# Performance work log

Measured on AMD Instinct MI355X. Metric: run time of the kernel, lower is better.

The kernel has to match this reference:

```python
import jax, jax.numpy as jnp
import numpy as np

E = 1024      # embed_dim
H = 16        # num_heads
D = E // H    # head_dim = 64
K = 4         # num_hyper_nodes
MAX_SEQ = 8192
ROPE_BASE = 10000.0
SCALE = D ** -0.5


def rotate_half(x):
    half = x.shape[-1] // 2
    return jnp.concatenate([-x[..., half:], x[..., :half]], axis=-1)


def _rope_cache():
    inv_freq = 1.0 / (ROPE_BASE ** (jnp.arange(0, D, 2, dtype=jnp.float32) / D))
    t = jnp.arange(MAX_SEQ, dtype=jnp.float32)
    freqs = jnp.outer(t, inv_freq)                       # (MAX_SEQ, D/2)
    emb = jnp.concatenate([freqs, freqs], axis=-1)       # (MAX_SEQ, D)
    return jnp.cos(emb), jnp.sin(emb)


def setup_inputs() -> dict:
    key = jax.random.key(0)
    ks = jax.random.split(key, 6)
    B, S = 2, 2048
    w_scale = E ** -0.5  # keep pre-softmax logits in a sane range
    return {
        "x":  jax.random.normal(ks[0], (B, S, E), dtype=jnp.float32),
        "Wq": jax.random.normal(ks[1], (E, E), dtype=jnp.float32) * w_scale,
        "Wk": jax.random.normal(ks[2], (E, E), dtype=jnp.float32) * w_scale,
        "Wv": jax.random.normal(ks[3], (E, E), dtype=jnp.float32) * w_scale,
        "Wr": jax.random.normal(ks[4], (E, H * K), dtype=jnp.float32) * w_scale,
        "Wo": jax.random.normal(ks[5], (E, E), dtype=jnp.float32) * w_scale,
    }


def reference(x, Wq, Wk, Wv, Wr, Wo):
    B, S, _ = x.shape
    # projections -> (B, H, S, D)
    q = (x @ Wq).reshape(B, S, H, D).transpose(0, 2, 1, 3)
    k = (x @ Wk).reshape(B, S, H, D).transpose(0, 2, 1, 3)
    v = (x @ Wv).reshape(B, S, H, D).transpose(0, 2, 1, 3)

    # node routing probabilities (B, H, S, K)
    logits = (x @ Wr).reshape(B, S, H, K).transpose(0, 2, 1, 3)
    node_probs = jax.nn.softmax(logits, axis=-1)

    # expected per-node position: sum_{j<i} p[j,k]  -> (B, H, S, K)
    expected_pos = jnp.cumsum(node_probs, axis=2) - node_probs

    # fractional-position RoPE via linear interpolation of the cos/sin cache
    cos_c, sin_c = _rope_cache()
    pos = jnp.clip(expected_pos, 0.0, MAX_SEQ - 1)
    pf = pos.astype(jnp.int32)                   # floor
    pc = jnp.minimum(pf + 1, MAX_SEQ - 1)        # ceil
    frac = (pos - pf.astype(pos.dtype))[..., None]
    cos = cos_c[pf] + frac * (cos_c[pc] - cos_c[pf])   # (B,H,S,K,D)
    sin = sin_c[pf] + frac * (sin_c[pc] - sin_c[pf])

    # Weighted combine over nodes. Since q_k = q*cos_k + rh(q)*sin_k is linear
    # in (cos_k, sin_k), sum_k p_k * q_k = q * (sum_k p_k cos_k) + rh(q) * (sum_k p_k sin_k)
    cos_w = jnp.einsum('bhsk,bhskd->bhsd', node_probs, cos)
    sin_w = jnp.einsum('bhsk,bhskd->bhsd', node_probs, sin)
    q_r = q * cos_w + rotate_half(q) * sin_w
    k_r = k * cos_w + rotate_half(k) * sin_w

    # P(same node) weights (B, H, S, S)
    node_w = jnp.einsum('bhik,bhjk->bhij', node_probs, node_probs)

    scores = jnp.einsum('bhid,bhjd->bhij', q_r, k_r) * SCALE
    scores = scores + jnp.log(node_w + 1e-8)
    causal = jnp.tril(jnp.ones((S, S), dtype=bool))
    scores = jnp.where(causal[None, None], scores, -jnp.inf)
    attn = jax.nn.softmax(scores, axis=-1)

    out = jnp.einsum('bhij,bhjd->bhid', attn, v)
    out = out.transpose(0, 2, 1, 3).reshape(B, S, E)
    return out @ Wo
```

## Files before the change

### kernel.cpp

```cpp
#include <hip/hip_runtime.h>

#define E_ 1024
#define H_ 16
#define D_ 64
#define K_ 4
#define S_ 2048
#define B_ 2
#define BS_ 4096
#define BH_ 32
#define CT_ 2080

typedef __attribute__((ext_vector_type(8))) short short8;
typedef __attribute__((ext_vector_type(4))) float f32x4;
typedef __attribute__((ext_vector_type(4))) unsigned short u16x4;

__device__ __forceinline__ unsigned short f2bf(float f) {
  union { float f; unsigned u; } v; v.f = f;
  unsigned r = v.u + 0x7FFFu + ((v.u >> 16) & 1u);
  return (unsigned short)(r >> 16);
}
__device__ __forceinline__ float bf2f(unsigned short u) {
  union { unsigned u; float f; } v; v.u = ((unsigned)u) << 16; return v.f;
}

typedef __attribute__((address_space(1))) const void gvoid;
typedef __attribute__((address_space(3))) void lvoid;
__device__ __forceinline__ void gload_lds16(const void* g, void* l) {
  __builtin_amdgcn_global_load_lds((gvoid*)g, (lvoid*)l, 16, 0, 0);
}

__device__ __forceinline__ short8 lds8(const unsigned short* base, int row, int chunk) {
  int off = row * 128 + (((chunk ^ (row & 7)) & 7) << 4);
  return *(const short8*)((const char*)base + off);
}

__device__ __forceinline__ float redmax16(float v) {
  int iv = __float_as_int(v);
  v = fmaxf(v, __int_as_float(__builtin_amdgcn_update_dpp(iv, iv, 0xB1, 0xF, 0xF, true)));
  iv = __float_as_int(v);
  v = fmaxf(v, __int_as_float(__builtin_amdgcn_update_dpp(iv, iv, 0x4E, 0xF, 0xF, true)));
  v = fmaxf(v, __shfl_xor(v, 4, 16));
  v = fmaxf(v, __shfl_xor(v, 8, 16));
  return v;
}

__global__ __launch_bounds__(256) void k_convert_x(const float* __restrict__ x,
                                                   unsigned short* __restrict__ xb) {
  int i = blockIdx.x * 256 + threadIdx.x;
  float4 v = ((const float4*)x)[i];
  u16x4 o; o.x = f2bf(v.x); o.y = f2bf(v.y); o.z = f2bf(v.z); o.w = f2bf(v.w);
  ((u16x4*)xb)[i] = o;
}

__global__ __launch_bounds__(256) void k_transpose_w(const float* __restrict__ Wq,
    const float* __restrict__ Wk, const float* __restrict__ Wv, const float* __restrict__ Wo,
    unsigned short* __restrict__ wt) {
  const float* W = blockIdx.z == 0 ? Wq : blockIdx.z == 1 ? Wk : blockIdx.z == 2 ? Wv : Wo;
  unsigned short* out = wt + (size_t)blockIdx.z * E_ * E_;
  __shared__ float tile[64][65];
  int k0 = blockIdx.y * 64, n0 = blockIdx.x * 64;
  int r = threadIdx.x >> 2, q4 = threadIdx.x & 3;
#pragma unroll
  for (int q = 0; q < 4; q++) {
    int c4 = q4 + q * 4;
    float4 v = *(const float4*)&W[(size_t)(k0 + r) * E_ + n0 + c4 * 4];
    tile[r][c4 * 4 + 0] = v.x; tile[r][c4 * 4 + 1] = v.y;
    tile[r][c4 * 4 + 2] = v.z; tile[r][c4 * 4 + 3] = v.w;
  }
  __syncthreads();
#pragma unroll
  for (int q = 0; q < 4; q++) {
    int cb = (q4 + q * 4) * 4;
    u16x4 o;
    o.x = f2bf(tile[cb + 0][r]); o.y = f2bf(tile[cb + 1][r]);
    o.z = f2bf(tile[cb + 2][r]); o.w = f2bf(tile[cb + 3][r]);
    *(u16x4*)&out[(size_t)(n0 + r) * E_ + k0 + cb] = o;
  }
}

__global__ __launch_bounds__(256) void k_cache(float* __restrict__ cosc, float* __restrict__ sinc) {
  int i = blockIdx.x * 256 + threadIdx.x;
  if (i >= CT_ * 32) return;
  int tt = i >> 5, f = i & 31;
  float invf = __expf(-(float)(2 * f) * (9.210340371976184f / 64.f));
  float ang = (float)tt * invf;
  cosc[i] = cosf(ang); sinc[i] = sinf(ang);
}

__global__ __launch_bounds__(256) void k_router(const float* __restrict__ x,
    const float* __restrict__ Wr, float* __restrict__ logits) {
  __shared__ float xs[2][16 * 16 * 4];
  __shared__ float ws[2][64 * 16 * 4];
  int t = threadIdx.x;
  int m0 = blockIdx.x * 16;
  int r = t >> 4, cq = t & 15;
  f32x4 acc = {0.f, 0.f, 0.f, 0.f};

  auto stage = [&](int chunk, int buf) {
    int e0 = chunk * 64;
    gload_lds16(x + (size_t)(m0 + (t >> 4)) * E_ + e0 + (((t & 15) ^ (t >> 4)) << 2),
                &xs[buf][(size_t)t * 4]);
#pragma unroll
    for (int j = 0; j < 4; j++) {
      int slot = j * 256 + t;
      gload_lds16(Wr + (size_t)(e0 + (slot >> 4)) * 64 + ((slot & 15) << 2),
                  &ws[buf][(size_t)slot * 4]);
    }
  };

  stage(0, 0);
  __syncthreads();
  for (int chunk = 0; chunk < 16; chunk++) {
    int cur = chunk & 1;
    if (chunk < 15) stage(chunk + 1, cur ^ 1);
#pragma unroll
    for (int e4 = 0; e4 < 16; e4++) {
      f32x4 xf = *(const f32x4*)&xs[cur][(r * 16 + (e4 ^ r)) * 4];
#pragma unroll
      for (int i = 0; i < 4; i++) {
        f32x4 wf = *(const f32x4*)&ws[cur][((e4 * 4 + i) * 16 + cq) * 4];
        acc[0] = fmaf(xf[i], wf[0], acc[0]);
        acc[1] = fmaf(xf[i], wf[1], acc[1]);
        acc[2] = fmaf(xf[i], wf[2], acc[2]);
        acc[3] = fmaf(xf[i], wf[3], acc[3]);
      }
    }
    __syncthreads();
  }
  *(f32x4*)&logits[(size_t)(m0 + r) * 64 + cq * 4] = acc;
}

__global__ __launch_bounds__(256) void k_scan(const float* __restrict__ logits,
    float* __restrict__ probs, unsigned short* __restrict__ pb, float* __restrict__ epos) {
  int bh = blockIdx.x; int b = bh >> 4, h = bh & 15;
  int t = threadIdx.x;
  float p[8][4];
  float own[4] = {0.f, 0.f, 0.f, 0.f};
#pragma unroll
  for (int r = 0; r < 8; r++) {
    int s = t * 8 + r;
    float4 lg = *(const float4*)&logits[(size_t)(b * S_ + s) * 64 + h * 4];
    float m = fmaxf(fmaxf(lg.x, lg.y), fmaxf(lg.z, lg.w));
    float e0 = __expf(lg.x - m), e1 = __expf(lg.y - m), e2 = __expf(lg.z - m), e3 = __expf(lg.w - m);
    float inv = 1.f / (e0 + e1 + e2 + e3);
    p[r][0] = e0 * inv; p[r][1] = e1 * inv; p[r][2] = e2 * inv; p[r][3] = e3 * inv;
    own[0] += p[r][0]; own[1] += p[r][1]; own[2] += p[r][2]; own[3] += p[r][3];
    float4 pv; pv.x = p[r][0]; pv.y = p[r][1]; pv.z = p[r][2]; pv.w = p[r][3];
    *(float4*)&probs[((size_t)bh * S_ + s) * 4] = pv;
    u16x4 pu; pu.x = f2bf(p[r][0]); pu.y = f2bf(p[r][1]);
    pu.z = f2bf(p[r][2]); pu.w = f2bf(p[r][3]);
    *(u16x4*)&pb[((size_t)bh * S_ + s) * 4] = pu;
  }
  __shared__ float sc[4][256];
#pragma unroll
  for (int k = 0; k < 4; k++) sc[k][t] = own[k];
  __syncthreads();
  for (int off = 1; off < 256; off <<= 1) {
    float v0 = 0, v1 = 0, v2 = 0, v3 = 0;
    if (t >= off) { v0 = sc[0][t - off]; v1 = sc[1][t - off]; v2 = sc[2][t - off]; v3 = sc[3][t - off]; }
    __syncthreads();
    if (t >= off) { sc[0][t] += v0; sc[1][t] += v1; sc[2][t] += v2; sc[3][t] += v3; }
    __syncthreads();
  }
  float run[4];
#pragma unroll
  for (int k = 0; k < 4; k++) run[k] = sc[k][t] - own[k];
#pragma unroll
  for (int r = 0; r < 8; r++) {
    int s = t * 8 + r;
    float4 ev; ev.x = run[0]; ev.y = run[1]; ev.z = run[2]; ev.w = run[3];
    *(float4*)&epos[((size_t)bh * S_ + s) * 4] = ev;
    run[0] += p[r][0]; run[1] += p[r][1]; run[2] += p[r][2]; run[3] += p[r][3];
  }
}

__global__ __launch_bounds__(256) void k_cwsw(const float* __restrict__ probs,
    const float* __restrict__ epos, const float* __restrict__ cosc, const float* __restrict__ sinc,
    float* __restrict__ cw, float* __restrict__ sw) {
  int bh = blockIdx.y;
  int s = blockIdx.x * 8 + (threadIdx.x >> 5);
  int f = threadIdx.x & 31;
  size_t row = (size_t)bh * S_ + s;
  float cacc = 0.f, sacc = 0.f;
#pragma unroll
  for (int k = 0; k < 4; k++) {
    float pk = probs[row * 4 + k];
    float pos = epos[row * 4 + k];
    pos = fminf(fmaxf(pos, 0.f), (float)(CT_ - 2));
    int pf = (int)pos; float fr = pos - (float)pf;
    float c0 = cosc[pf * 32 + f], c1 = cosc[pf * 32 + 32 + f];
    float s0 = sinc[pf * 32 + f], s1 = sinc[pf * 32 + 32 + f];
    cacc = fmaf(pk, c0 + fr * (c1 - c0), cacc);
    sacc = fmaf(pk, s0 + fr * (s1 - s0), sacc);
  }
  cw[row * 32 + f] = cacc; sw[row * 32 + f] = sacc;
}

__device__ __forceinline__ void gemm_128x128(const unsigned short* __restrict__ A,
    const unsigned short* __restrict__ Bt, int m0, int n0,
    unsigned short* lA, unsigned short* lB, f32x4 acc[4][4]) {
  int t = threadIdx.x, w = t >> 6, lane = t & 63;
  int wm = w >> 1, wn = w & 1;
  int arow = lane & 15, agrp = lane >> 4;
  for (int k0 = 0; k0 < E_; k0 += 64) {
    __syncthreads();
#pragma unroll
    for (int j = 0; j < 4; j++) {
      int c = j * 256 + w * 64 + lane;
      int row = c >> 3, slot = c & 7;
      gload_lds16(A + (size_t)(m0 + row) * E_ + k0 + ((slot ^ (row & 7)) << 3),
                  lA + (size_t)(j * 256 + w * 64) * 8);
      gload_lds16(Bt + (size_t)(n0 + row) * E_ + k0 + ((slot ^ (row & 7)) << 3),
                  lB + (size_t)(j * 256 + w * 64) * 8);
    }
    __syncthreads();
#pragma unroll
    for (int ks = 0; ks < 2; ks++) {
      short8 af[4], bfr[4];
#pragma unroll
      for (int mi = 0; mi < 4; mi++) af[mi] = lds8(lA, wm * 64 + mi * 16 + arow, ks * 4 + agrp);
#pragma unroll
      for (int nj = 0; nj < 4; nj++) bfr[nj] = lds8(lB, wn * 64 + nj * 16 + arow, ks * 4 + agrp);
#pragma unroll
      for (int mi = 0; mi < 4; mi++)
#pragma unroll
        for (int nj = 0; nj < 4; nj++)
          acc[mi][nj] = __builtin_amdgcn_mfma_f32_16x16x32_bf16(af[mi], bfr[nj], acc[mi][nj], 0, 0, 0);
    }
  }
}

__global__ __launch_bounds__(256) void k_gemm_qkv(const unsigned short* __restrict__ xb,
    const unsigned short* __restrict__ wt, const float* __restrict__ cw, const float* __restrict__ sw,
    unsigned short* __restrict__ qr, unsigned short* __restrict__ kr, unsigned short* __restrict__ vb) {
  __shared__ unsigned short lA[128 * 64], lB[128 * 64];
  int z = blockIdx.z;
  int m0 = blockIdx.y * 128, n0 = blockIdx.x * 128;
  f32x4 acc[4][4];
  f32x4 zero4 = {0.f, 0.f, 0.f, 0.f};
#pragma unroll
  for (int a = 0; a < 4; a++)
#pragma unroll
    for (int b2 = 0; b2 < 4; b2++) acc[a][b2] = zero4;
  gemm_128x128(xb, wt + (size_t)z * E_ * E_, m0, n0, lA, lB, acc);

  int t = threadIdx.x, w = t >> 6, lane = t & 63;
  int wm = w >> 1, wn = w & 1;
  int arow = lane & 15, agrp = lane >> 4;
  if (z == 2) {
#pragma unroll
    for (int mi = 0; mi < 4; mi++) {
      int i0 = m0 + wm * 64 + mi * 16 + agrp * 4;
      int b = i0 >> 11, s0 = i0 & 2047;
#pragma unroll
      for (int nj = 0; nj < 4; nj++) {
        int col = n0 + wn * 64 + nj * 16 + arow;
        int h = col >> 6, dl = col & 63;
        u16x4 o;
        o.x = f2bf(acc[mi][nj][0]); o.y = f2bf(acc[mi][nj][1]);
        o.z = f2bf(acc[mi][nj][2]); o.w = f2bf(acc[mi][nj][3]);
        *(u16x4*)&vb[((size_t)(b * H_ + h) * 64 + dl) * S_ + s0] = o;
      }
    }
  } else {
    unsigned short* out = (z == 0) ? qr : kr;
    float scl = (z == 0) ? 0.18033688011f : 1.0f;
    int h = (n0 + wn * 64) >> 6;
#pragma unroll
    for (int mi = 0; mi < 4; mi++)
#pragma unroll
      for (int reg = 0; reg < 4; reg++) {
        int i = m0 + wm * 64 + mi * 16 + agrp * 4 + reg;
        int b = i >> 11, s = i & 2047;
        size_t rbase = (size_t)(b * H_ + h) * S_ + s;
        float cw0 = cw[rbase * 32 + arow], cw1 = cw[rbase * 32 + 16 + arow];
        float sw0 = sw[rbase * 32 + arow], sw1 = sw[rbase * 32 + 16 + arow];
#pragma unroll
        for (int nj = 0; nj < 4; nj++) {
          float v = acc[mi][nj][reg];
          float part = acc[mi][nj ^ 2][reg];
          float rh = (nj < 2) ? -part : part;
          float cwv = (nj & 1) ? cw1 : cw0;
          float swv = (nj & 1) ? sw1 : sw0;
          out[rbase * 64 + nj * 16 + arow] = f2bf((v * cwv + rh * swv) * scl);
        }
      }
  }
}

__global__ __launch_bounds__(256) void k_gemm_out(const unsigned short* __restrict__ ob,
    const unsigned short* __restrict__ wot, float* __restrict__ dout) {
  __shared__ unsigned short lA[64 * 64];
  __shared__ unsigned short lB[128 * 64];
  int m0 = blockIdx.y * 64, n0 = blockIdx.x * 128;
  int t = threadIdx.x, w = t >> 6, lane = t & 63;
  int arow = lane & 15, agrp = lane >> 4;
  f32x4 acc[4][2];
  f32x4 zero4 = {0.f, 0.f, 0.f, 0.f};
#pragma unroll
  for (int a = 0; a < 4; a++) { acc[a][0] = zero4; acc[a][1] = zero4; }
  for (int k0 = 0; k0 < E_; k0 += 64) {
    __syncthreads();
#pragma unroll
    for (int j = 0; j < 2; j++) {
      int c = j * 256 + t;
      int row = c >> 3, slot = c & 7;
      gload_lds16(ob + (size_t)(m0 + row) * E_ + k0 + ((slot ^ (row & 7)) << 3),
                  lA + (size_t)c * 8);
    }
#pragma unroll
    for (int j = 0; j < 4; j++) {
      int c = j * 256 + t;
      int row = c >> 3, slot = c & 7;
      gload_lds16(wot + (size_t)(n0 + row) * E_ + k0 + ((slot ^ (row & 7)) << 3),
                  lB + (size_t)c * 8);
    }
    __syncthreads();
#pragma unroll
    for (int ks = 0; ks < 2; ks++) {
      short8 af[4], bfr[2];
#pragma unroll
      for (int mi = 0; mi < 4; mi++) af[mi] = lds8(lA, mi * 16 + arow, ks * 4 + agrp);
#pragma unroll
      for (int nj = 0; nj < 2; nj++) bfr[nj] = lds8(lB, w * 32 + nj * 16 + arow, ks * 4 + agrp);
#pragma unroll
      for (int mi = 0; mi < 4; mi++)
#pragma unroll
        for (int nj = 0; nj < 2; nj++)
          acc[mi][nj] = __builtin_amdgcn_mfma_f32_16x16x32_bf16(af[mi], bfr[nj], acc[mi][nj], 0, 0, 0);
    }
  }
#pragma unroll
  for (int mi = 0; mi < 4; mi++)
#pragma unroll
    for (int reg = 0; reg < 4; reg++) {
      int i = m0 + mi * 16 + agrp * 4 + reg;
#pragma unroll
      for (int nj = 0; nj < 2; nj++) {
        int col = n0 + w * 32 + nj * 16 + arow;
        dout[(size_t)i * E_ + col] = acc[mi][nj][reg];
      }
    }
}

__device__ const int4 kChunk[38] = {
  { 8,0, 8, 8},{ 8,9,17, 9},{12,0, 8,19},{12,9,17,20},
  { 7,0, 7, 6},{ 7,8,15, 7},{10,0, 7,13},{11,0, 7,16},{11,8,15,17},{11,16,23,18},
  {12,18,25,21},{14,0, 7,26},{14,8,15,27},{15,0, 7,30},{15,8,15,31},{15,16,23,32},
  {15,24,31,33},{ 3,0, 7,-1},
  { 6,0, 6, 4},{ 6,7,13, 5},{ 9,0, 6,10},{ 9,7,13,11},{10,8,14,14},{10,15,21,15},
  {13,0, 6,22},{13,7,13,23},{13,14,20,24},{13,21,27,25},{14,16,22,28},{14,23,29,29},
  { 5,0, 5, 2},{ 5,6,11, 3},{ 9,14,19,12},{ 2,0, 5,-1},
  { 4,0, 4, 0},{ 4,5, 9, 1},{ 1,0, 3,-1},{ 0,0, 1,-1}
};

__device__ __forceinline__ short8 mkfrag(u16x4 pv) {
  union { u16x4 v; unsigned u[2]; } pun; pun.v = pv;
  union { short8 s; unsigned u[4]; } z;
  z.u[0] = pun.u[0]; z.u[1] = pun.u[1]; z.u[2] = 0; z.u[3] = 0;
  return z.s;
}

__device__ __forceinline__ void qk_phase2(const char* lKc, const short8 qf[2][2],
    const int kOff[2][4], f32x4 zero4, f32x4 sacc[2][4]) {
#pragma unroll
  for (int ct = 0; ct < 4; ct++) {
    short8 kf = *(const short8*)(lKc + kOff[0][ct]);
    sacc[0][ct] = __builtin_amdgcn_mfma_f32_16x16x32_bf16(qf[0][0], kf, zero4, 0, 0, 0);
    sacc[1][ct] = __builtin_amdgcn_mfma_f32_16x16x32_bf16(qf[1][0], kf, zero4, 0, 0, 0);
  }
#pragma unroll
  for (int ct = 0; ct < 4; ct++) {
    short8 kf = *(const short8*)(lKc + kOff[1][ct]);
    sacc[0][ct] = __builtin_amdgcn_mfma_f32_16x16x32_bf16(qf[0][1], kf, sacc[0][ct], 0, 0, 0);
    sacc[1][ct] = __builtin_amdgcn_mfma_f32_16x16x32_bf16(qf[1][1], kf, sacc[1][ct], 0, 0, 0);
  }
}

__device__ __forceinline__ void softmax_half(const f32x4 sacc[4], const short8 piF,
    const short8 pjF[4], char* lPh, int kv0, int ig_base, int arow, int agrp,
    const int wOff[4][4], float mrow[4], f32x4 oacc[4], f32x4& o4) {
  f32x4 eps4 = {1e-8f, 1e-8f, 1e-8f, 1e-8f};
  f32x4 nwa[4];
#pragma unroll
  for (int ct = 0; ct < 4; ct++)
    nwa[ct] = __builtin_amdgcn_mfma_f32_16x16x32_bf16(piF, pjF[ct], eps4, 0, 0, 0);
  float sv[4][4];
  float rmax[4];
  if (kv0 + 63 > ig_base) {
#pragma unroll
    for (int ct = 0; ct < 4; ct++) {
      int jg = kv0 + ct * 16 + arow;
#pragma unroll
      for (int reg = 0; reg < 4; reg++) {
        int ig = ig_base + agrp * 4 + reg;
        float xv = sacc[ct][reg];
        if (jg > ig) xv = -1e30f;
        sv[ct][reg] = xv;
      }
    }
  } else {
#pragma unroll
    for (int ct = 0; ct < 4; ct++)
#pragma unroll
      for (int reg = 0; reg < 4; reg++)
        sv[ct][reg] = sacc[ct][reg];
  }
#pragma unroll
  for (int reg = 0; reg < 4; reg++)
    rmax[reg] = redmax16(fmaxf(fmaxf(sv[0][reg], sv[1][reg]), fmaxf(sv[2][reg], sv[3][reg])));
  bool ok = (rmax[0] <= mrow[0] + 11.5f) & (rmax[1] <= mrow[1] + 11.5f) &
            (rmax[2] <= mrow[2] + 11.5f) & (rmax[3] <= mrow[3] + 11.5f);
  if (!__all(ok)) {
    float alpha[4];
#pragma unroll
    for (int reg = 0; reg < 4; reg++) {
      float mn = fmaxf(mrow[reg], rmax[reg]);
      alpha[reg] = __builtin_amdgcn_exp2f(mrow[reg] - mn);
      mrow[reg] = mn;
    }
#pragma unroll
    for (int dt = 0; dt < 4; dt++) {
      f32x4 o = oacc[dt];
      o.x *= alpha[0]; o.y *= alpha[1]; o.z *= alpha[2]; o.w *= alpha[3];
      oacc[dt] = o;
    }
    o4.x *= alpha[0]; o4.y *= alpha[1]; o4.z *= alpha[2]; o4.w *= alpha[3];
  }
#pragma unroll
  for (int ct = 0; ct < 4; ct++)
#pragma unroll
    for (int reg = 0; reg < 4; reg++)
      sv[ct][reg] = __builtin_amdgcn_exp2f(sv[ct][reg] - mrow[reg]) * nwa[ct][reg];
#pragma unroll
  for (int ct = 0; ct < 4; ct++) {
#pragma unroll
    for (int rp = 0; rp < 2; rp++) {
      unsigned pk;
      asm("v_cvt_pk_bf16_f32 %0, %1, %2" : "=v"(pk) : "v"(sv[ct][rp * 2]), "v"(sv[ct][rp * 2 + 1]));
      *(unsigned short*)(lPh + wOff[ct][rp * 2 + 0]) = (unsigned short)pk;
      *(unsigned short*)(lPh + wOff[ct][rp * 2 + 1]) = (unsigned short)(pk >> 16);
    }
  }
}

__device__ __forceinline__ void pv2(const char* lPw, const char* lVc,
    const int pOff[2], const int kOff[2][4], f32x4 oacc0[4], f32x4 oacc1[4],
    f32x4& o40, f32x4& o41) {
  const short8 ones = {16256, 16256, 16256, 16256, 16256, 16256, 16256, 16256};
#pragma unroll
  for (int ks = 0; ks < 2; ks++) {
    short8 pf0 = *(const short8*)(lPw + pOff[ks]);
    short8 pf1 = *(const short8*)(lPw + 2048 + pOff[ks]);
    o40 = __builtin_amdgcn_mfma_f32_16x16x32_bf16(pf0, ones, o40, 0, 0, 0);
    o41 = __builtin_amdgcn_mfma_f32_16x16x32_bf16(pf1, ones, o41, 0, 0, 0);
#pragma unroll
    for (int dt = 0; dt < 4; dt++) {
      short8 vf = *(const short8*)(lVc + kOff[ks][dt]);
      oacc0[dt] = __builtin_amdgcn_mfma_f32_16x16x32_bf16(pf0, vf, oacc0[dt], 0, 0, 0);
      oacc1[dt] = __builtin_amdgcn_mfma_f32_16x16x32_bf16(pf1, vf, oacc1[dt], 0, 0, 0);
    }
  }
}

__global__ __launch_bounds__(256, 2) void k_attn(const unsigned short* __restrict__ qr,
    const unsigned short* __restrict__ kr, const unsigned short* __restrict__ vb,
    const unsigned short* __restrict__ pb, unsigned short* __restrict__ ob,
    unsigned short* __restrict__ ObP, float* __restrict__ ml) {
  __shared__ unsigned short lK[2][64 * 64];
  __shared__ unsigned short lV[2][64 * 64];
  __shared__ unsigned short lP[4][2][16 * 64];
  int id = blockIdx.x;
  int xcd = id & 7, slt = id >> 3;
  int bh = xcd * 4 + (slt & 3);
  int4 ck = kChunk[slt >> 2];
  int qt2 = ck.x, j0 = ck.y, j1 = ck.z, part = ck.w;
  int t = threadIdx.x, w = t >> 6, lane = t & 63;
  int arow = lane & 15, agrp = lane >> 4;
  int q0 = qt2 * 128;
  size_t base = (size_t)bh * S_ * 64;
  size_t bhS = (size_t)bh * S_;

  int kOff[2][4], pOff[2], wOff[4][4];
#pragma unroll
  for (int ks = 0; ks < 2; ks++) {
    pOff[ks] = arow * 128 + (((ks * 4 + agrp) ^ (arow & 7)) << 4);
#pragma unroll
    for (int ct = 0; ct < 4; ct++) {
      int row = ct * 16 + arow;
      kOff[ks][ct] = row * 128 + (((ks * 4 + agrp) ^ (row & 7)) << 4);
    }
  }
#pragma unroll
  for (int ct = 0; ct < 4; ct++) {
    int col2 = (ct * 16 + arow) * 2;
#pragma unroll
    for (int rr = 0; rr < 4; rr++) {
      int r = agrp * 4 + rr;
      wOff[ct][rr] = r * 128 + (col2 ^ ((r & 7) << 4));
    }
  }

  const unsigned short* kSrc[2];
  const unsigned short* vSrc[2];
  unsigned short* kDst[2];
  unsigned short* vDst[2];
#pragma unroll
  for (int j = 0; j < 2; j++) {
    int c = j * 256 + w * 64 + lane;
    int row = c >> 3, slot = c & 7;
    kSrc[j] = kr + base + (size_t)row * 64 + ((slot ^ (row & 7)) << 3);
    vSrc[j] = vb + base + (size_t)row * S_ + ((slot ^ (row & 7)) << 3);
    kDst[j] = &lK[0][(j * 256 + w * 64) * 8];
    vDst[j] = &lV[0][(j * 256 + w * 64) * 8];
  }
  const unsigned short* pjSrc[4];
#pragma unroll
  for (int ct = 0; ct < 4; ct++) pjSrc[ct] = pb + (bhS + ct * 16 + arow) * 4;

  short8 qf[2][2];
  short8 piF[2];
  float mrow[2][4];
  f32x4 oacc[2][4];
  f32x4 o4[2];
  f32x4 zero4 = {0.f, 0.f, 0.f, 0.f};
#pragma unroll
  for (int hh = 0; hh < 2; hh++) {
#pragma unroll
    for (int ks = 0; ks < 2; ks++)
      qf[hh][ks] = *(const short8*)&qr[base + (size_t)(q0 + hh * 64 + w * 16 + arow) * 64 + ks * 32 + agrp * 8];
    u16x4 pv = {0, 0, 0, 0};
    if (agrp == 0) pv = *(const u16x4*)&pb[(bhS + q0 + hh * 64 + w * 16 + arow) * 4];
    piF[hh] = mkfrag(pv);
#pragma unroll
    for (int reg = 0; reg < 4; reg++) mrow[hh][reg] = -1e30f;
#pragma unroll
    for (int dt = 0; dt < 4; dt++) oacc[hh][dt] = zero4;
    o4[hh] = zero4;
  }

  auto stageK = [&](int jt, int buf) {
#pragma unroll
    for (int j = 0; j < 2; j++)
      gload_lds16(kSrc[j] + jt * 4096, kDst[j] + buf * 4096);
  };
  auto stageV = [&](int jt, int buf) {
#pragma unroll
    for (int j = 0; j < 2; j++)
      gload_lds16(vSrc[j] + jt * 64, vDst[j] + buf * 4096);
  };
  auto loadPj = [&](int jt, u16x4 pj[4]) {
#pragma unroll
    for (int ct = 0; ct < 4; ct++) {
      u16x4 z = {0, 0, 0, 0};
      if (agrp == 0) z = *(const u16x4*)(pjSrc[ct] + jt * 256);
      pj[ct] = z;
    }
  };

  u16x4 pjv[4], pjvn[4];
  stageK(j0, 0);
  stageV(j0, 0);
  loadPj(j0, pjv);
  __syncthreads();

  char* lPw = (char*)&lP[w][0][0];
  int nt = j1 - j0 + 1;
  for (int i = 0; i < nt; i++) {
    int cur = i & 1;
    int kv0 = (j0 + i) * 64;
    bool hn = (i + 1) < nt;
    if (hn) {
      stageK(j0 + i + 1, cur ^ 1);
      stageV(j0 + i + 1, cur ^ 1);
    }

    f32x4 sacc[2][4];
    __builtin_amdgcn_s_setprio(1);
    qk_phase2((const char*)lK + cur * 8192, qf, kOff, zero4, sacc);
    __builtin_amdgcn_s_setprio(0);

    short8 pjF[4];
#pragma unroll
    for (int ct = 0; ct < 4; ct++) pjF[ct] = mkfrag(pjv[ct]);
#pragma unroll
    for (int hh = 0; hh < 2; hh++)
      softmax_half(sacc[hh], piF[hh], pjF, lPw + hh * 2048, kv0, q0 + hh * 64 + w * 16,
                   arow, agrp, wOff, mrow[hh], oacc[hh], o4[hh]);

    if (hn) loadPj(j0 + i + 1, pjvn);

    asm volatile("s_waitcnt lgkmcnt(0)" ::: "memory");
    __builtin_amdgcn_sched_barrier(0);
    __builtin_amdgcn_s_setprio(1);
    pv2(lPw, (const char*)lV + cur * 8192, pOff, kOff, oacc[0], oacc[1], o4[0], o4[1]);
    __builtin_amdgcn_s_setprio(0);
    if (hn) {
#pragma unroll
      for (int ct = 0; ct < 4; ct++) pjv[ct] = pjvn[ct];
    }
    __syncthreads();
  }

  if (part >= 0) {
    unsigned short* Op = ObP + ((size_t)bh * 34 + part) * 8192;
    float* mlp = ml + ((size_t)bh * 34 + part) * 256;
#pragma unroll
    for (int hh = 0; hh < 2; hh++) {
#pragma unroll
      for (int dt = 0; dt < 4; dt++)
#pragma unroll
        for (int reg = 0; reg < 4; reg++) {
          int row = hh * 64 + w * 16 + agrp * 4 + reg;
          Op[row * 64 + dt * 16 + arow] = f2bf(oacc[hh][dt][reg]);
        }
      if (arow == 0) {
#pragma unroll
        for (int reg = 0; reg < 4; reg++) {
          int row = hh * 64 + w * 16 + agrp * 4 + reg;
          mlp[row] = mrow[hh][reg];
          mlp[128 + row] = o4[hh][reg];
        }
      }
    }
  } else {
    int b = bh >> 4, h8 = bh & 15;
#pragma unroll
    for (int hh = 0; hh < 2; hh++) {
      f32x4 inv4;
      inv4.x = 1.f / o4[hh].x; inv4.y = 1.f / o4[hh].y;
      inv4.z = 1.f / o4[hh].z; inv4.w = 1.f / o4[hh].w;
#pragma unroll
      for (int dt = 0; dt < 4; dt++)
#pragma unroll
        for (int reg = 0; reg < 4; reg++) {
          int i = q0 + hh * 64 + w * 16 + agrp * 4 + reg;
          int d = dt * 16 + arow;
          float v = oacc[hh][dt][reg] * inv4[reg];
          ob[((size_t)(b * S_ + i) * H_ + h8) * 64 + d] = f2bf(v);
        }
    }
  }
}

__global__ __launch_bounds__(256) void k_merge(const unsigned short* __restrict__ ObP,
    const float* __restrict__ ml, unsigned short* __restrict__ ob) {
  int qx = blockIdx.x, bh = blockIdx.y;
  int qt2 = 4 + qx;
  int np = qt2 <= 8 ? 2 : (qt2 <= 12 ? 3 : 4);
  int bslot = qt2 <= 8 ? (qt2 - 4) * 2 : (qt2 <= 12 ? 10 + (qt2 - 9) * 3 : 22 + (qt2 - 13) * 4);
  int t = threadIdx.x;
  int r = t >> 1, dh = (t & 1) * 32;
  float mp[4], lp[4];
  float m = -1e30f;
  for (int p2 = 0; p2 < np; p2++) {
    const float* mlp = ml + ((size_t)bh * 34 + bslot + p2) * 256;
    mp[p2] = mlp[r]; lp[p2] = mlp[128 + r];
    m = fmaxf(m, mp[p2]);
  }
  float a[4], l = 0.f;
  for (int p2 = 0; p2 < np; p2++) { a[p2] = __builtin_amdgcn_exp2f(mp[p2] - m); l = fmaf(lp[p2], a[p2], l); }
  float inv = 1.f / l;
  for (int p2 = 0; p2 < np; p2++) a[p2] *= inv;
  int i = qt2 * 128 + r, b = bh >> 4, h = bh & 15;
  unsigned short* op = ob + ((size_t)(b * S_ + i) * H_ + h) * 64 + dh;
#pragma unroll
  for (int q = 0; q < 8; q++) {
    float a0 = 0.f, a1 = 0.f, a2 = 0.f, a3 = 0.f;
    for (int p2 = 0; p2 < np; p2++) {
      const unsigned short* Op = ObP + ((size_t)bh * 34 + bslot + p2) * 8192 + r * 64 + dh + q * 4;
      u16x4 xx = *(const u16x4*)Op;
      a0 = fmaf(bf2f(xx.x), a[p2], a0);
      a1 = fmaf(bf2f(xx.y), a[p2], a1);
      a2 = fmaf(bf2f(xx.z), a[p2], a2);
      a3 = fmaf(bf2f(xx.w), a[p2], a3);
    }
    u16x4 o; o.x = f2bf(a0); o.y = f2bf(a1); o.z = f2bf(a2); o.w = f2bf(a3);
    *(u16x4*)(op + q * 4) = o;
  }
}

extern "C" void kernel_launch(void* const* d_in, const int* in_sizes, int n_in,
                              void* d_out, int out_size, void* d_ws, size_t ws_size,
                              hipStream_t stream) {
  const float* x  = (const float*)d_in[0];
  const float* Wq = (const float*)d_in[1];
  const float* Wk = (const float*)d_in[2];
  const float* Wv = (const float*)d_in[3];
  const float* Wr = (const float*)d_in[4];
  const float* Wo = (const float*)d_in[5];
  float* dout = (float*)d_out;

  char* p = (char*)d_ws;
  auto alloc = [&](size_t bytes) -> char* {
    char* r = p; p += (bytes + 255) & ~(size_t)255; return r;
  };
  unsigned short* xb   = (unsigned short*)alloc((size_t)BS_ * E_ * 2);
  unsigned short* wt   = (unsigned short*)alloc((size_t)4 * E_ * E_ * 2);
  float* cosc          = (float*)alloc((size_t)CT_ * 32 * 4);
  float* sinc          = (float*)alloc((size_t)CT_ * 32 * 4);
  float* probs         = (float*)alloc((size_t)BH_ * S_ * 4 * 4);
  unsigned short* pb   = (unsigned short*)alloc((size_t)BH_ * S_ * 4 * 2);
  float* logits        = (float*)alloc((size_t)BS_ * 64 * 4);
  float* epos          = (float*)alloc((size_t)BH_ * S_ * 4 * 4);
  float* cw            = (float*)alloc((size_t)BH_ * S_ * 32 * 4);
  float* sw            = (float*)alloc((size_t)BH_ * S_ * 32 * 4);
  unsigned short* qrb  = (unsigned short*)alloc((size_t)BH_ * S_ * 64 * 2);
  unsigned short* krb  = (unsigned short*)alloc((size_t)BH_ * S_ * 64 * 2);
  unsigned short* vbb  = (unsigned short*)alloc((size_t)BH_ * S_ * 64 * 2);
  unsigned short* obb  = (unsigned short*)alloc((size_t)BS_ * E_ * 2);
  if ((size_t)(p - (char*)d_ws) > ws_size) return;

  unsigned short* ObP = (unsigned short*)logits;
  float* mlbuf = (float*)xb;

  k_convert_x<<<BS_ * E_ / 4 / 256, 256, 0, stream>>>(x, xb);
  k_transpose_w<<<dim3(16, 16, 4), 256, 0, stream>>>(Wq, Wk, Wv, Wo, wt);
  k_cache<<<(CT_ * 32 + 255) / 256, 256, 0, stream>>>(cosc, sinc);
  k_router<<<BS_ / 16, 256, 0, stream>>>(x, Wr, logits);
  k_scan<<<BH_, 256, 0, stream>>>(logits, probs, pb, epos);
  k_cwsw<<<dim3(S_ / 8, BH_), 256, 0, stream>>>(probs, epos, cosc, sinc, cw, sw);
  k_gemm_qkv<<<dim3(8, 32, 3), 256, 0, stream>>>(xb, wt, cw, sw, qrb, krb, vbb);
  k_attn<<<dim3(38 * BH_), 256, 0, stream>>>(qrb, krb, vbb, pb, obb, ObP, mlbuf);
  k_merge<<<dim3(12, BH_), 256, 0, stream>>>(ObP, mlbuf, obb);
  k_gemm_out<<<dim3(8, 64), 256, 0, stream>>>(obb, wt + (size_t)3 * E_ * E_, dout);
}
```

Before: 192.3 us.

## Merge prep kernels into one launch and split scan into chunked two-pass

Four independent preprocessing kernels (x conversion, weight transpose, RoPE cache, router GEMM) are merged into a single launch that dispatches on block index, removing launch gaps and letting them run concurrently. The single-block-per-head scan is replaced by a chunked scan over 256 blocks plus a tiny pass that computes chunk bases, which k_cwsw adds back when it reads positions. This trades the low-parallelism scan (32 blocks) for an extra tiny launch and a larger LDS footprint in the merged kernel, which may reduce occupancy for the simple branches.

```diff
diff --git a/kernel.cpp b/kernel.cpp
--- a/kernel.cpp
+++ b/kernel.cpp
@@ -44,116 +44,123 @@
   return v;
 }
 
-__global__ __launch_bounds__(256) void k_convert_x(const float* __restrict__ x,
-                                                   unsigned short* __restrict__ xb) {
-  int i = blockIdx.x * 256 + threadIdx.x;
-  float4 v = ((const float4*)x)[i];
-  u16x4 o; o.x = f2bf(v.x); o.y = f2bf(v.y); o.z = f2bf(v.z); o.w = f2bf(v.w);
-  ((u16x4*)xb)[i] = o;
-}
-
-__global__ __launch_bounds__(256) void k_transpose_w(const float* __restrict__ Wq,
-    const float* __restrict__ Wk, const float* __restrict__ Wv, const float* __restrict__ Wo,
-    unsigned short* __restrict__ wt) {
-  const float* W = blockIdx.z == 0 ? Wq : blockIdx.z == 1 ? Wk : blockIdx.z == 2 ? Wv : Wo;
-  unsigned short* out = wt + (size_t)blockIdx.z * E_ * E_;
-  __shared__ float tile[64][65];
-  int k0 = blockIdx.y * 64, n0 = blockIdx.x * 64;
-  int r = threadIdx.x >> 2, q4 = threadIdx.x & 3;
-#pragma unroll
-  for (int q = 0; q < 4; q++) {
-    int c4 = q4 + q * 4;
-    float4 v = *(const float4*)&W[(size_t)(k0 + r) * E_ + n0 + c4 * 4];
-    tile[r][c4 * 4 + 0] = v.x; tile[r][c4 * 4 + 1] = v.y;
-    tile[r][c4 * 4 + 2] = v.z; tile[r][c4 * 4 + 3] = v.w;
-  }
-  __syncthreads();
-#pragma unroll
-  for (int q = 0; q < 4; q++) {
-    int cb = (q4 + q * 4) * 4;
-    u16x4 o;
-    o.x = f2bf(tile[cb + 0][r]); o.y = f2bf(tile[cb + 1][r]);
-    o.z = f2bf(tile[cb + 2][r]); o.w = f2bf(tile[cb + 3][r]);
-    *(u16x4*)&out[(size_t)(n0 + r) * E_ + k0 + cb] = o;
-  }
-}
-
-__global__ __launch_bounds__(256) void k_cache(float* __restrict__ cosc, float* __restrict__ sinc) {
-  int i = blockIdx.x * 256 + threadIdx.x;
-  if (i >= CT_ * 32) return;
-  int tt = i >> 5, f = i & 31;
-  float invf = __expf(-(float)(2 * f) * (9.210340371976184f / 64.f));
-  float ang = (float)tt * invf;
-  cosc[i] = cosf(ang); sinc[i] = sinf(ang);
-}
-
-__global__ __launch_bounds__(256) void k_router(const float* __restrict__ x,
-    const float* __restrict__ Wr, float* __restrict__ logits) {
-  __shared__ float xs[2][16 * 16 * 4];
-  __shared__ float ws[2][64 * 16 * 4];
+__global__ __launch_bounds__(256) void k_prep(const float* __restrict__ x,
+    const float* __restrict__ Wq, const float* __restrict__ Wk, const float* __restrict__ Wv,
+    const float* __restrict__ Wo, const float* __restrict__ Wr,
+    unsigned short* __restrict__ xb, unsigned short* __restrict__ wt,
+    float* __restrict__ cosc, float* __restrict__ sinc, float* __restrict__ logits) {
+  __shared__ __align__(16) char smem[40960];
+  int blk = blockIdx.x;
   int t = threadIdx.x;
-  int m0 = blockIdx.x * 16;
-  int r = t >> 4, cq = t & 15;
-  f32x4 acc = {0.f, 0.f, 0.f, 0.f};
-
-  auto stage = [&](int chunk, int buf) {
-    int e0 = chunk * 64;
-    gload_lds16(x + (size_t)(m0 + (t >> 4)) * E_ + e0 + (((t & 15) ^ (t >> 4)) << 2),
-                &xs[buf][(size_t)t * 4]);
-#pragma unroll
-    for (int j = 0; j < 4; j++) {
-      int slot = j * 256 + t;
-      gload_lds16(Wr + (size_t)(e0 + (slot >> 4)) * 64 + ((slot & 15) << 2),
-                  &ws[buf][(size_t)slot * 4]);
-    }
-  };
-
-  stage(0, 0);
-  __syncthreads();
-  for (int chunk = 0; chunk < 16; chunk++) {
-    int cur = chunk & 1;
-    if (chunk < 15) stage(chunk + 1, cur ^ 1);
-#pragma unroll
-    for (int e4 = 0; e4 < 16; e4++) {
-      f32x4 xf = *(const f32x4*)&xs[cur][(r * 16 + (e4 ^ r)) * 4];
-#pragma unroll
-      for (int i = 0; i < 4; i++) {
-        f32x4 wf = *(const f32x4*)&ws[cur][((e4 * 4 + i) * 16 + cq) * 4];
-        acc[0] = fmaf(xf[i], wf[0], acc[0]);
-        acc[1] = fmaf(xf[i], wf[1], acc[1]);
-        acc[2] = fmaf(xf[i], wf[2], acc[2]);
-        acc[3] = fmaf(xf[i], wf[3], acc[3]);
+
+  if (blk < 4096) {
+    int i = blk * 256 + t;
+    float4 v = ((const float4*)x)[i];
+    u16x4 o; o.x = f2bf(v.x); o.y = f2bf(v.y); o.z = f2bf(v.z); o.w = f2bf(v.w);
+    ((u16x4*)xb)[i] = o;
+    return;
+  }
+  blk -= 4096;
+  if (blk < 1024) {
+    int z = blk >> 8, rem = blk & 255;
+    int k0 = (rem >> 4) * 64, n0 = (rem & 15) * 64;
+    const float* W = z == 0 ? Wq : z == 1 ? Wk : z == 2 ? Wv : Wo;
+    unsigned short* out = wt + (size_t)z * E_ * E_;
+    float (*tile)[65] = (float(*)[65])smem;
+    int r = t >> 2, q4 = t & 3;
+#pragma unroll
+    for (int q = 0; q < 4; q++) {
+      int c4 = q4 + q * 4;
+      float4 v = *(const float4*)&W[(size_t)(k0 + r) * E_ + n0 + c4 * 4];
+      tile[r][c4 * 4 + 0] = v.x; tile[r][c4 * 4 + 1] = v.y;
+      tile[r][c4 * 4 + 2] = v.z; tile[r][c4 * 4 + 3] = v.w;
+    }
+    __syncthreads();
+#pragma unroll
+    for (int q = 0; q < 4; q++) {
+      int cb = (q4 + q * 4) * 4;
+      u16x4 o;
+      o.x = f2bf(tile[cb + 0][r]); o.y = f2bf(tile[cb + 1][r]);
+      o.z = f2bf(tile[cb + 2][r]); o.w = f2bf(tile[cb + 3][r]);
+      *(u16x4*)&out[(size_t)(n0 + r) * E_ + k0 + cb] = o;
+    }
+    return;
+  }
+  blk -= 1024;
+  if (blk < 260) {
+    int i = blk * 256 + t;
+    if (i < CT_ * 32) {
+      int tt = i >> 5, f = i & 31;
+      float invf = __expf(-(float)(2 * f) * (9.210340371976184f / 64.f));
+      float ang = (float)tt * invf;
+      cosc[i] = cosf(ang); sinc[i] = sinf(ang);
+    }
+    return;
+  }
+  blk -= 260;
+  {
+    float* xs = (float*)smem;
+    float* ws = xs + 2048;
+    int m0 = blk * 16;
+    int r = t >> 4, cq = t & 15;
+    f32x4 acc = {0.f, 0.f, 0.f, 0.f};
+
+    auto stage = [&](int chunk, int buf) {
+      int e0 = chunk * 64;
+      gload_lds16(x + (size_t)(m0 + (t >> 4)) * E_ + e0 + (((t & 15) ^ (t >> 4)) << 2),
+                  xs + buf * 1024 + t * 4);
+#pragma unroll
+      for (int j = 0; j < 4; j++) {
+        int slot = j * 256 + t;
+        gload_lds16(Wr + (size_t)(e0 + (slot >> 4)) * 64 + ((slot & 15) << 2),
+                    ws + buf * 4096 + slot * 4);
       }
-    }
-    __syncthreads();
-  }
-  *(f32x4*)&logits[(size_t)(m0 + r) * 64 + cq * 4] = acc;
-}
-
-__global__ __launch_bounds__(256) void k_scan(const float* __restrict__ logits,
-    float* __restrict__ probs, unsigned short* __restrict__ pb, float* __restrict__ epos) {
-  int bh = blockIdx.x; int b = bh >> 4, h = bh & 15;
+    };
+
+    stage(0, 0);
+    __syncthreads();
+    for (int chunk = 0; chunk < 16; chunk++) {
+      int cur = chunk & 1;
+      if (chunk < 15) stage(chunk + 1, cur ^ 1);
+#pragma unroll
+      for (int e4 = 0; e4 < 16; e4++) {
+        f32x4 xf = *(const f32x4*)(xs + cur * 1024 + (r * 16 + (e4 ^ r)) * 4);
+#pragma unroll
+        for (int i = 0; i < 4; i++) {
+          f32x4 wf = *(const f32x4*)(ws + cur * 4096 + ((e4 * 4 + i) * 16 + cq) * 4);
+          acc[0] = fmaf(xf[i], wf[0], acc[0]);
+          acc[1] = fmaf(xf[i], wf[1], acc[1]);
+          acc[2] = fmaf(xf[i], wf[2], acc[2]);
+          acc[3] = fmaf(xf[i], wf[3], acc[3]);
+        }
+      }
+      __syncthreads();
+    }
+    *(f32x4*)&logits[(size_t)(m0 + r) * 64 + cq * 4] = acc;
+  }
+}
+
+__global__ __launch_bounds__(256) void k_scan1(const float* __restrict__ logits,
+    float* __restrict__ probs, unsigned short* __restrict__ pb, float* __restrict__ eposl,
+    float* __restrict__ chunkSum) {
+  int g = blockIdx.x;
+  int bh = g >> 3, c = g & 7;
+  int b = bh >> 4, h = bh & 15;
   int t = threadIdx.x;
-  float p[8][4];
-  float own[4] = {0.f, 0.f, 0.f, 0.f};
-#pragma unroll
-  for (int r = 0; r < 8; r++) {
-    int s = t * 8 + r;
-    float4 lg = *(const float4*)&logits[(size_t)(b * S_ + s) * 64 + h * 4];
-    float m = fmaxf(fmaxf(lg.x, lg.y), fmaxf(lg.z, lg.w));
-    float e0 = __expf(lg.x - m), e1 = __expf(lg.y - m), e2 = __expf(lg.z - m), e3 = __expf(lg.w - m);
-    float inv = 1.f / (e0 + e1 + e2 + e3);
-    p[r][0] = e0 * inv; p[r][1] = e1 * inv; p[r][2] = e2 * inv; p[r][3] = e3 * inv;
-    own[0] += p[r][0]; own[1] += p[r][1]; own[2] += p[r][2]; own[3] += p[r][3];
-    float4 pv; pv.x = p[r][0]; pv.y = p[r][1]; pv.z = p[r][2]; pv.w = p[r][3];
-    *(float4*)&probs[((size_t)bh * S_ + s) * 4] = pv;
-    u16x4 pu; pu.x = f2bf(p[r][0]); pu.y = f2bf(p[r][1]);
-    pu.z = f2bf(p[r][2]); pu.w = f2bf(p[r][3]);
-    *(u16x4*)&pb[((size_t)bh * S_ + s) * 4] = pu;
-  }
+  int s = c * 256 + t;
+  float4 lg = *(const float4*)&logits[(size_t)(b * S_ + s) * 64 + h * 4];
+  float m = fmaxf(fmaxf(lg.x, lg.y), fmaxf(lg.z, lg.w));
+  float e0 = __expf(lg.x - m), e1 = __expf(lg.y - m), e2 = __expf(lg.z - m), e3 = __expf(lg.w - m);
+  float inv = 1.f / (e0 + e1 + e2 + e3);
+  float p[4] = {e0 * inv, e1 * inv, e2 * inv, e3 * inv};
+  float4 pv; pv.x = p[0]; pv.y = p[1]; pv.z = p[2]; pv.w = p[3];
+  *(float4*)&probs[((size_t)bh * S_ + s) * 4] = pv;
+  u16x4 pu; pu.x = f2bf(p[0]); pu.y = f2bf(p[1]); pu.z = f2bf(p[2]); pu.w = f2bf(p[3]);
+  *(u16x4*)&pb[((size_t)bh * S_ + s) * 4] = pu;
+
   __shared__ float sc[4][256];
 #pragma unroll
-  for (int k = 0; k < 4; k++) sc[k][t] = own[k];
+  for (int k = 0; k < 4; k++) sc[k][t] = p[k];
   __syncthreads();
   for (int off = 1; off < 256; off <<= 1) {
     float v0 = 0, v1 = 0, v2 = 0, v3 = 0;
@@ -162,30 +169,43 @@
     if (t >= off) { sc[0][t] += v0; sc[1][t] += v1; sc[2][t] += v2; sc[3][t] += v3; }
     __syncthreads();
   }
-  float run[4];
-#pragma unroll
-  for (int k = 0; k < 4; k++) run[k] = sc[k][t] - own[k];
-#pragma unroll
-  for (int r = 0; r < 8; r++) {
-    int s = t * 8 + r;
-    float4 ev; ev.x = run[0]; ev.y = run[1]; ev.z = run[2]; ev.w = run[3];
-    *(float4*)&epos[((size_t)bh * S_ + s) * 4] = ev;
-    run[0] += p[r][0]; run[1] += p[r][1]; run[2] += p[r][2]; run[3] += p[r][3];
+  float4 ev;
+  ev.x = sc[0][t] - p[0]; ev.y = sc[1][t] - p[1];
+  ev.z = sc[2][t] - p[2]; ev.w = sc[3][t] - p[3];
+  *(float4*)&eposl[((size_t)bh * S_ + s) * 4] = ev;
+  if (t == 255) {
+    float4 cs; cs.x = sc[0][255]; cs.y = sc[1][255]; cs.z = sc[2][255]; cs.w = sc[3][255];
+    *(float4*)&chunkSum[(size_t)(bh * 8 + c) * 4] = cs;
+  }
+}
+
+__global__ __launch_bounds__(64) void k_scan2(const float* __restrict__ chunkSum,
+    float* __restrict__ chunkBase) {
+  int bh = threadIdx.x;
+  if (bh >= 32) return;
+  float r0 = 0.f, r1 = 0.f, r2 = 0.f, r3 = 0.f;
+  for (int c = 0; c < 8; c++) {
+    float4 cs = *(const float4*)&chunkSum[(size_t)(bh * 8 + c) * 4];
+    float4 cb; cb.x = r0; cb.y = r1; cb.z = r2; cb.w = r3;
+    *(float4*)&chunkBase[(size_t)(bh * 8 + c) * 4] = cb;
+    r0 += cs.x; r1 += cs.y; r2 += cs.z; r3 += cs.w;
   }
 }
 
 __global__ __launch_bounds__(256) void k_cwsw(const float* __restrict__ probs,
-    const float* __restrict__ epos, const float* __restrict__ cosc, const float* __restrict__ sinc,
+    const float* __restrict__ eposl, const float* __restrict__ chunkBase,
+    const float* __restrict__ cosc, const float* __restrict__ sinc,
     float* __restrict__ cw, float* __restrict__ sw) {
   int bh = blockIdx.y;
   int s = blockIdx.x * 8 + (threadIdx.x >> 5);
   int f = threadIdx.x & 31;
   size_t row = (size_t)bh * S_ + s;
+  const float* cb = &chunkBase[(size_t)(bh * 8 + (s >> 8)) * 4];
   float cacc = 0.f, sacc = 0.f;
 #pragma unroll
   for (int k = 0; k < 4; k++) {
     float pk = probs[row * 4 + k];
-    float pos = epos[row * 4 + k];
+    float pos = eposl[row * 4 + k] + cb[k];
     pos = fminf(fmaxf(pos, 0.f), (float)(CT_ - 2));
     int pf = (int)pos; float fr = pos - (float)pf;
     float c0 = cosc[pf * 32 + f], c1 = cosc[pf * 32 + 32 + f];
@@ -709,17 +729,18 @@
   unsigned short* krb  = (unsigned short*)alloc((size_t)BH_ * S_ * 64 * 2);
   unsigned short* vbb  = (unsigned short*)alloc((size_t)BH_ * S_ * 64 * 2);
   unsigned short* obb  = (unsigned short*)alloc((size_t)BS_ * E_ * 2);
+  float* chunkSum      = (float*)alloc((size_t)BH_ * 8 * 4 * 4);
+  float* chunkBase     = (float*)alloc((size_t)BH_ * 8 * 4 * 4);
   if ((size_t)(p - (char*)d_ws) > ws_size) return;
 
   unsigned short* ObP = (unsigned short*)logits;
   float* mlbuf = (float*)xb;
 
-  k_convert_x<<<BS_ * E_ / 4 / 256, 256, 0, stream>>>(x, xb);
-  k_transpose_w<<<dim3(16, 16, 4), 256, 0, stream>>>(Wq, Wk, Wv, Wo, wt);
-  k_cache<<<(CT_ * 32 + 255) / 256, 256, 0, stream>>>(cosc, sinc);
-  k_router<<<BS_ / 16, 256, 0, stream>>>(x, Wr, logits);
-  k_scan<<<BH_, 256, 0, stream>>>(logits, probs, pb, epos);
-  k_cwsw<<<dim3(S_ / 8, BH_), 256, 0, stream>>>(probs, epos, cosc, sinc, cw, sw);
+  k_prep<<<4096 + 1024 + 260 + 256, 256, 0, stream>>>(x, Wq, Wk, Wv, Wo, Wr,
+                                                      xb, wt, cosc, sinc, logits);
+  k_scan1<<<BH_ * 8, 256, 0, stream>>>(logits, probs, pb, epos, chunkSum);
+  k_scan2<<<1, 64, 0, stream>>>(chunkSum, chunkBase);
+  k_cwsw<<<dim3(S_ / 8, BH_), 256, 0, stream>>>(probs, epos, chunkBase, cosc, sinc, cw, sw);
   k_gemm_qkv<<<dim3(8, 32, 3), 256, 0, stream>>>(xb, wt, cw, sw, qrb, krb, vbb);
   k_attn<<<dim3(38 * BH_), 256, 0, stream>>>(qrb, krb, vbb, pb, obb, ObP, mlbuf);
   k_merge<<<dim3(12, BH_), 256, 0, stream>>>(ObP, mlbuf, obb);
```

New measurement: 191.6 us. No clear change (-0.4%).
